# Kernel optimization log

Measured on AMD Instinct MI355X. Metric: run time of the kernel, lower is better.

Reference implementation:

```python
import jax, jax.numpy as jnp
import numpy as np

SCALE = 0.08838834764831845  # 1/sqrt(head_dim=128)


def setup_inputs() -> dict:
    key = jax.random.key(0)
    ks = jax.random.split(key, 5)
    B, H, D = 16, 8, 128          # batch (decode seqs), kv heads, head_dim
    BS, BPS = 16, 128             # block_size, blocks per sequence
    NBLK = B * BPS                # total cache blocks (2048)
    CTX = 2048                    # context length per sequence
    q = jax.random.normal(ks[0], (B, H, D), jnp.float32)
    k = jax.random.normal(ks[1], (B, H, D), jnp.float32)
    v = jax.random.normal(ks[2], (B, H, D), jnp.float32)
    k_cache = jax.random.normal(ks[3], (NBLK, BS, H, D), jnp.float32)
    v_cache = jax.random.normal(ks[4], (NBLK, BS, H, D), jnp.float32)
    # each sequence owns a distinct contiguous set of blocks
    block_tables = jnp.arange(B * BPS, dtype=jnp.int32).reshape(B, BPS)
    context_lens = jnp.full((B,), CTX, dtype=jnp.int32)
    # slot for the newest token (position CTX-1) of each sequence
    last = CTX - 1
    slot_mapping = block_tables[:, last // BS] * BS + (last % BS)
    return {"q": q, "k": k, "v": v, "k_cache": k_cache, "v_cache": v_cache,
            "slot_mapping": slot_mapping.astype(jnp.int32),
            "block_tables": block_tables, "context_lens": context_lens}


def reference(q, k, v, k_cache, v_cache, slot_mapping, block_tables, context_lens):
    # ---- store_kvcache: scatter new k/v tokens into paged caches ----
    nblk, bs, H, D = k_cache.shape
    k_cache = k_cache.reshape(nblk * bs, H, D).at[slot_mapping].set(k).reshape(nblk, bs, H, D)
    v_cache = v_cache.reshape(nblk * bs, H, D).at[slot_mapping].set(v).reshape(nblk, bs, H, D)

    # ---- _sdpa_decode: paged gather + masked attention (q_per_seq = 1) ----
    B, nb = block_tables.shape
    T = nb * bs                              # max tokens per sequence
    token_idx = jnp.arange(T, dtype=jnp.int32)
    block_idx = token_idx // bs
    token_off = token_idx % bs
    block_ids = block_tables[:, block_idx]   # [B, T]
    k_all = k_cache[block_ids, token_off]    # [B, T, H, D]
    v_all = v_cache[block_ids, token_off]    # [B, T, H, D]

    valid = token_idx[None, :] < context_lens[:, None]           # [B, T]
    q_pos = context_lens - 1                                     # q_per_seq == 1
    causal = token_idx[None, :] <= q_pos[:, None]                # [B, T]
    mask = valid & causal

    scores = jnp.einsum("bhd,bthd->bht", q, k_all) * SCALE       # [B, H, T]
    scores = jnp.where(mask[:, None, :], scores, -jnp.inf)
    p = jax.nn.softmax(scores, axis=-1)
    out = jnp.einsum("bht,bthd->bhd", p, v_all)                  # [B, H, D]
    return out
```

## Files before the change

### kernel.cpp

```cpp
#include <hip/hip_runtime.h>
#include <math.h>

#define B_ 16
#define H_ 8
#define D_ 128
#define BS_ 16
#define BPS_ 128
#define T_ (BPS_ * BS_)
#define ROW_ (H_ * D_)
#define SCALE_ 0.08838834764831845f

template<int NS>
__global__ __launch_bounds__(256) void attn_partial(
    const float* __restrict__ q,
    const float* __restrict__ knew,
    const float* __restrict__ vnew,
    const float* __restrict__ kc,
    const float* __restrict__ vc,
    const int* __restrict__ btab,
    const int* __restrict__ clen,
    float* __restrict__ ws_m,
    float* __restrict__ ws_l,
    float* __restrict__ ws_o)
{
    constexpr int CHUNK = T_ / NS;
    constexpr int TPW = CHUNK / 4;
    constexpr int NBLK_C = CHUNK / BS_;

    const int c = blockIdx.x;
    const int b = blockIdx.y;
    const int tid = threadIdx.x;
    const int wave = tid >> 6;
    const int lane = tid & 63;
    const int hl = lane & 31;
    const int half = lane >> 5;
    const int ctx = clen[b];
    const int cs = c * CHUNK;

    __shared__ int   s_bt[NBLK_C];
    __shared__ float s_p[H_][CHUNK];
    __shared__ float s_mx[H_], s_l[H_];
    __shared__ float s_o[4][H_][D_];

    if (tid < NBLK_C) s_bt[tid] = btab[b * BPS_ + c * NBLK_C + tid];

    float4 q4[4];
    #pragma unroll
    for (int j = 0; j < 4; ++j)
        q4[j] = *(const float4*)(q + (size_t)b * ROW_ + j * 256 + half * 128 + 4 * hl);
    __syncthreads();

    #pragma unroll 4
    for (int i = 0; i < TPW; i += 2) {
        float4 k4[8];
        #pragma unroll
        for (int u = 0; u < 2; ++u) {
            const int t = wave * TPW + i + u;
            const int tg = cs + t;
            const int blk = s_bt[t >> 4];
            const float* rb = (tg == ctx - 1)
                ? (knew + (size_t)b * ROW_)
                : (kc + ((size_t)blk * BS_ + (tg & 15)) * ROW_);
            #pragma unroll
            for (int j = 0; j < 4; ++j)
                k4[u * 4 + j] = *(const float4*)(rb + j * 256 + half * 128 + 4 * hl);
        }
        #pragma unroll
        for (int u = 0; u < 2; ++u) {
            const int t = wave * TPW + i + u;
            const int tg = cs + t;
            #pragma unroll
            for (int j = 0; j < 4; ++j) {
                const float4 kv = k4[u * 4 + j];
                float s = q4[j].x * kv.x + q4[j].y * kv.y + q4[j].z * kv.z + q4[j].w * kv.w;
                s += __shfl_xor(s, 16);
                s += __shfl_xor(s, 8);
                s += __shfl_xor(s, 4);
                s += __shfl_xor(s, 2);
                s += __shfl_xor(s, 1);
                if (hl == 0) s_p[2 * j + half][t] = (tg < ctx) ? s * SCALE_ : -INFINITY;
            }
        }
    }
    __syncthreads();

    {
        const int h = tid >> 5;
        float m = -INFINITY;
        for (int t = hl; t < CHUNK; t += 32) m = fmaxf(m, s_p[h][t]);
        m = fmaxf(m, __shfl_xor(m, 16));
        m = fmaxf(m, __shfl_xor(m, 8));
        m = fmaxf(m, __shfl_xor(m, 4));
        m = fmaxf(m, __shfl_xor(m, 2));
        m = fmaxf(m, __shfl_xor(m, 1));
        if (hl == 0) s_mx[h] = fmaxf(m, -1e30f);
    }
    __syncthreads();
    {
        const int h = tid >> 5;
        const float mx = s_mx[h];
        float l = 0.f;
        for (int t = hl; t < CHUNK; t += 32) {
            const float p = __expf(s_p[h][t] - mx);
            s_p[h][t] = p;
            l += p;
        }
        l += __shfl_xor(l, 16);
        l += __shfl_xor(l, 8);
        l += __shfl_xor(l, 4);
        l += __shfl_xor(l, 2);
        l += __shfl_xor(l, 1);
        if (hl == 0) s_l[h] = l;
    }
    __syncthreads();

    float4 acc[4];
    #pragma unroll
    for (int j = 0; j < 4; ++j) acc[j] = make_float4(0.f, 0.f, 0.f, 0.f);
    #pragma unroll 4
    for (int i = 0; i < TPW; i += 2) {
        float4 v4[8];
        #pragma unroll
        for (int u = 0; u < 2; ++u) {
            const int t = wave * TPW + i + u;
            const int tg = cs + t;
            const int blk = s_bt[t >> 4];
            const float* rb = (tg == ctx - 1)
                ? (vnew + (size_t)b * ROW_)
                : (vc + ((size_t)blk * BS_ + (tg & 15)) * ROW_);
            #pragma unroll
            for (int j = 0; j < 4; ++j)
                v4[u * 4 + j] = *(const float4*)(rb + j * 256 + half * 128 + 4 * hl);
        }
        #pragma unroll
        for (int u = 0; u < 2; ++u) {
            const int t = wave * TPW + i + u;
            #pragma unroll
            for (int j = 0; j < 4; ++j) {
                const float pw = s_p[2 * j + half][t];
                acc[j].x += pw * v4[u * 4 + j].x;
                acc[j].y += pw * v4[u * 4 + j].y;
                acc[j].z += pw * v4[u * 4 + j].z;
                acc[j].w += pw * v4[u * 4 + j].w;
            }
        }
    }
    #pragma unroll
    for (int j = 0; j < 4; ++j)
        *(float4*)&s_o[wave][2 * j + half][4 * hl] = acc[j];
    __syncthreads();

    for (int r = tid; r < H_ * D_; r += 256) {
        const int h = r >> 7, d = r & 127;
        const float oo = s_o[0][h][d] + s_o[1][h][d] + s_o[2][h][d] + s_o[3][h][d];
        ws_o[((size_t)(b * H_ + h) * NS + c) * D_ + d] = oo;
    }
    if (tid < H_) {
        ws_m[(b * H_ + tid) * NS + c] = s_mx[tid];
        ws_l[(b * H_ + tid) * NS + c] = s_l[tid];
    }
}

template<int NS>
__global__ __launch_bounds__(128) void attn_reduce(
    const float* __restrict__ ws_m,
    const float* __restrict__ ws_l,
    const float* __restrict__ ws_o,
    float* __restrict__ out)
{
    const int bh = blockIdx.x;
    const int tid = threadIdx.x;

    __shared__ float s_co[NS];
    __shared__ float s_lg;

    if (tid < 64) {
        float m = -INFINITY;
        for (int cc = tid; cc < NS; cc += 64) m = fmaxf(m, ws_m[bh * NS + cc]);
        m = fmaxf(m, __shfl_xor(m, 32));
        m = fmaxf(m, __shfl_xor(m, 16));
        m = fmaxf(m, __shfl_xor(m, 8));
        m = fmaxf(m, __shfl_xor(m, 4));
        m = fmaxf(m, __shfl_xor(m, 2));
        m = fmaxf(m, __shfl_xor(m, 1));
        float lw = 0.f;
        for (int cc = tid; cc < NS; cc += 64) {
            const float co = __expf(ws_m[bh * NS + cc] - m);
            s_co[cc] = co;
            lw += ws_l[bh * NS + cc] * co;
        }
        lw += __shfl_xor(lw, 32);
        lw += __shfl_xor(lw, 16);
        lw += __shfl_xor(lw, 8);
        lw += __shfl_xor(lw, 4);
        lw += __shfl_xor(lw, 2);
        lw += __shfl_xor(lw, 1);
        if (tid == 0) s_lg = lw;
    }
    __syncthreads();

    float acc = 0.f;
    #pragma unroll 8
    for (int cc = 0; cc < NS; ++cc)
        acc += s_co[cc] * ws_o[((size_t)bh * NS + cc) * D_ + tid];
    out[(size_t)bh * D_ + tid] = acc / s_lg;
}

template<int NS>
static void launch_all(const float* q, const float* knew, const float* vnew,
                       const float* kc, const float* vc,
                       const int* btab, const int* clen,
                       float* ws, float* out, hipStream_t stream)
{
    float* ws_m = ws;
    float* ws_l = ws + B_ * H_ * NS;
    float* ws_o = ws + 2 * B_ * H_ * NS;
    attn_partial<NS><<<dim3(NS, B_), 256, 0, stream>>>(q, knew, vnew, kc, vc,
                                                       btab, clen, ws_m, ws_l, ws_o);
    attn_reduce<NS><<<dim3(B_ * H_), 128, 0, stream>>>(ws_m, ws_l, ws_o, out);
}

extern "C" void kernel_launch(void* const* d_in, const int* in_sizes, int n_in,
                              void* d_out, int out_size, void* d_ws, size_t ws_size,
                              hipStream_t stream) {
    const float* q    = (const float*)d_in[0];
    const float* knew = (const float*)d_in[1];
    const float* vnew = (const float*)d_in[2];
    const float* kc   = (const float*)d_in[3];
    const float* vc   = (const float*)d_in[4];
    const int* btab = (const int*)d_in[6];
    const int* clen = (const int*)d_in[7];
    float* out = (float*)d_out;
    float* ws  = (float*)d_ws;

    const size_t need64 = (size_t)B_ * H_ * 64 * (2 + D_) * sizeof(float);
    const size_t need32 = (size_t)B_ * H_ * 32 * (2 + D_) * sizeof(float);
    if (ws_size >= need64)      launch_all<64>(q, knew, vnew, kc, vc, btab, clen, ws, out, stream);
    else if (ws_size >= need32) launch_all<32>(q, knew, vnew, kc, vc, btab, clen, ws, out, stream);
    else                        launch_all<16>(q, knew, vnew, kc, vc, btab, clen, ws, out, stream);
}
```

Baseline: 290.5 us.

## Restructure paged decode attention to keep scores in registers and prefetch V

Remaps threads so each group of 8 lanes owns one head, which shrinks the dot-product shuffle reduction to three steps. Scores now stay in registers and probabilities are recomputed on the fly instead of written back to shared memory. The first V tile is prefetched before the softmax barriers, and the max and sum passes are merged, with fewer barriers overall. It also adds a 128-way split when the workspace allows it and sets an occupancy hint in launch bounds. The cost is higher register pressure from fully unrolled score arrays and direct block-table loads from global memory.

```diff
diff --git a/kernel.cpp b/kernel.cpp
--- a/kernel.cpp
+++ b/kernel.cpp
@@ -11,7 +11,7 @@
 #define SCALE_ 0.08838834764831845f
 
 template<int NS>
-__global__ __launch_bounds__(256) void attn_partial(
+__global__ __launch_bounds__(256, 4) void attn_partial(
     const float* __restrict__ q,
     const float* __restrict__ knew,
     const float* __restrict__ vnew,
@@ -25,135 +25,163 @@
 {
     constexpr int CHUNK = T_ / NS;
     constexpr int TPW = CHUNK / 4;
-    constexpr int NBLK_C = CHUNK / BS_;
+    static_assert(TPW % 4 == 0 || TPW == 4, "TPW multiple of 4");
+    constexpr int NB = TPW / 4;
 
     const int c = blockIdx.x;
     const int b = blockIdx.y;
     const int tid = threadIdx.x;
     const int wave = tid >> 6;
     const int lane = tid & 63;
-    const int hl = lane & 31;
-    const int half = lane >> 5;
+    const int h = lane >> 3;
+    const int e = (lane & 7) * 4;
     const int ctx = clen[b];
     const int cs = c * CHUNK;
-
-    __shared__ int   s_bt[NBLK_C];
-    __shared__ float s_p[H_][CHUNK];
+    const int t0 = wave * TPW;
+
+    __shared__ float s_p[H_][CHUNK + 1];
     __shared__ float s_mx[H_], s_l[H_];
-    __shared__ float s_o[4][H_][D_];
-
-    if (tid < NBLK_C) s_bt[tid] = btab[b * BPS_ + c * NBLK_C + tid];
+    __shared__ float s_o[4][H_ * D_];
 
     float4 q4[4];
     #pragma unroll
-    for (int j = 0; j < 4; ++j)
-        q4[j] = *(const float4*)(q + (size_t)b * ROW_ + j * 256 + half * 128 + 4 * hl);
-    __syncthreads();
-
-    #pragma unroll 4
-    for (int i = 0; i < TPW; i += 2) {
-        float4 k4[8];
-        #pragma unroll
-        for (int u = 0; u < 2; ++u) {
-            const int t = wave * TPW + i + u;
+    for (int i = 0; i < 4; ++i)
+        q4[i] = *(const float4*)(q + (size_t)b * ROW_ + h * 128 + i * 32 + e);
+
+    float sc[TPW];
+
+    #pragma unroll
+    for (int bt = 0; bt < NB; ++bt) {
+        float4 kb[4][4];
+        #pragma unroll
+        for (int u = 0; u < 4; ++u) {
+            const int t = t0 + bt * 4 + u;
             const int tg = cs + t;
-            const int blk = s_bt[t >> 4];
+            const int blk = btab[b * BPS_ + (tg >> 4)];
             const float* rb = (tg == ctx - 1)
                 ? (knew + (size_t)b * ROW_)
-                : (kc + ((size_t)blk * BS_ + (tg & 15)) * ROW_);
-            #pragma unroll
-            for (int j = 0; j < 4; ++j)
-                k4[u * 4 + j] = *(const float4*)(rb + j * 256 + half * 128 + 4 * hl);
-        }
-        #pragma unroll
-        for (int u = 0; u < 2; ++u) {
-            const int t = wave * TPW + i + u;
+                : (kc + ((size_t)blk * BS_ + (t & 15)) * ROW_);
+            #pragma unroll
+            for (int i = 0; i < 4; ++i)
+                kb[u][i] = *(const float4*)(rb + h * 128 + i * 32 + e);
+        }
+        #pragma unroll
+        for (int u = 0; u < 4; ++u) {
+            const int t = t0 + bt * 4 + u;
             const int tg = cs + t;
-            #pragma unroll
-            for (int j = 0; j < 4; ++j) {
-                const float4 kv = k4[u * 4 + j];
-                float s = q4[j].x * kv.x + q4[j].y * kv.y + q4[j].z * kv.z + q4[j].w * kv.w;
-                s += __shfl_xor(s, 16);
-                s += __shfl_xor(s, 8);
-                s += __shfl_xor(s, 4);
-                s += __shfl_xor(s, 2);
-                s += __shfl_xor(s, 1);
-                if (hl == 0) s_p[2 * j + half][t] = (tg < ctx) ? s * SCALE_ : -INFINITY;
-            }
-        }
-    }
-    __syncthreads();
+            float s = 0.f;
+            #pragma unroll
+            for (int i = 0; i < 4; ++i)
+                s += q4[i].x * kb[u][i].x + q4[i].y * kb[u][i].y
+                   + q4[i].z * kb[u][i].z + q4[i].w * kb[u][i].w;
+            s += __shfl_xor(s, 1);
+            s += __shfl_xor(s, 2);
+            s += __shfl_xor(s, 4);
+            s = (tg < ctx) ? s * SCALE_ : -INFINITY;
+            sc[bt * 4 + u] = s;
+            if ((lane & 7) == 0) s_p[h][t] = s;
+        }
+    }
+
+    float4 vb0[4][4];
+    #pragma unroll
+    for (int u = 0; u < 4; ++u) {
+        const int t = t0 + u;
+        const int tg = cs + t;
+        const int blk = btab[b * BPS_ + (tg >> 4)];
+        const float* rb = (tg == ctx - 1)
+            ? (vnew + (size_t)b * ROW_)
+            : (vc + ((size_t)blk * BS_ + (t & 15)) * ROW_);
+        #pragma unroll
+        for (int i = 0; i < 4; ++i)
+            vb0[u][i] = *(const float4*)(rb + h * 128 + i * 32 + e);
+    }
+
+    asm volatile("s_waitcnt lgkmcnt(0)" ::: "memory");
+    __builtin_amdgcn_s_barrier();
+    __builtin_amdgcn_sched_barrier(0);
 
     {
-        const int h = tid >> 5;
+        const int hh = tid >> 5;
+        const int j = tid & 31;
         float m = -INFINITY;
-        for (int t = hl; t < CHUNK; t += 32) m = fmaxf(m, s_p[h][t]);
+        for (int t = j; t < CHUNK; t += 32) m = fmaxf(m, s_p[hh][t]);
         m = fmaxf(m, __shfl_xor(m, 16));
         m = fmaxf(m, __shfl_xor(m, 8));
         m = fmaxf(m, __shfl_xor(m, 4));
         m = fmaxf(m, __shfl_xor(m, 2));
         m = fmaxf(m, __shfl_xor(m, 1));
-        if (hl == 0) s_mx[h] = fmaxf(m, -1e30f);
-    }
-    __syncthreads();
-    {
-        const int h = tid >> 5;
-        const float mx = s_mx[h];
+        m = fmaxf(m, -1e30f);
         float l = 0.f;
-        for (int t = hl; t < CHUNK; t += 32) {
-            const float p = __expf(s_p[h][t] - mx);
-            s_p[h][t] = p;
-            l += p;
-        }
+        for (int t = j; t < CHUNK; t += 32) l += __expf(s_p[hh][t] - m);
         l += __shfl_xor(l, 16);
         l += __shfl_xor(l, 8);
         l += __shfl_xor(l, 4);
         l += __shfl_xor(l, 2);
         l += __shfl_xor(l, 1);
-        if (hl == 0) s_l[h] = l;
-    }
-    __syncthreads();
+        if (j == 0) { s_mx[hh] = m; s_l[hh] = l; }
+    }
+
+    asm volatile("s_waitcnt lgkmcnt(0)" ::: "memory");
+    __builtin_amdgcn_s_barrier();
+    __builtin_amdgcn_sched_barrier(0);
+
+    const float mx = s_mx[h];
 
     float4 acc[4];
     #pragma unroll
-    for (int j = 0; j < 4; ++j) acc[j] = make_float4(0.f, 0.f, 0.f, 0.f);
-    #pragma unroll 4
-    for (int i = 0; i < TPW; i += 2) {
-        float4 v4[8];
-        #pragma unroll
-        for (int u = 0; u < 2; ++u) {
-            const int t = wave * TPW + i + u;
+    for (int i = 0; i < 4; ++i) acc[i] = make_float4(0.f, 0.f, 0.f, 0.f);
+
+    #pragma unroll
+    for (int u = 0; u < 4; ++u) {
+        const float pw = __expf(sc[u] - mx);
+        #pragma unroll
+        for (int i = 0; i < 4; ++i) {
+            acc[i].x += pw * vb0[u][i].x;
+            acc[i].y += pw * vb0[u][i].y;
+            acc[i].z += pw * vb0[u][i].z;
+            acc[i].w += pw * vb0[u][i].w;
+        }
+    }
+    #pragma unroll
+    for (int bt = 1; bt < NB; ++bt) {
+        float4 vb[4][4];
+        #pragma unroll
+        for (int u = 0; u < 4; ++u) {
+            const int t = t0 + bt * 4 + u;
             const int tg = cs + t;
-            const int blk = s_bt[t >> 4];
+            const int blk = btab[b * BPS_ + (tg >> 4)];
             const float* rb = (tg == ctx - 1)
                 ? (vnew + (size_t)b * ROW_)
-                : (vc + ((size_t)blk * BS_ + (tg & 15)) * ROW_);
-            #pragma unroll
-            for (int j = 0; j < 4; ++j)
-                v4[u * 4 + j] = *(const float4*)(rb + j * 256 + half * 128 + 4 * hl);
-        }
-        #pragma unroll
-        for (int u = 0; u < 2; ++u) {
-            const int t = wave * TPW + i + u;
-            #pragma unroll
-            for (int j = 0; j < 4; ++j) {
-                const float pw = s_p[2 * j + half][t];
-                acc[j].x += pw * v4[u * 4 + j].x;
-                acc[j].y += pw * v4[u * 4 + j].y;
-                acc[j].z += pw * v4[u * 4 + j].z;
-                acc[j].w += pw * v4[u * 4 + j].w;
+                : (vc + ((size_t)blk * BS_ + (t & 15)) * ROW_);
+            #pragma unroll
+            for (int i = 0; i < 4; ++i)
+                vb[u][i] = *(const float4*)(rb + h * 128 + i * 32 + e);
+        }
+        #pragma unroll
+        for (int u = 0; u < 4; ++u) {
+            const float pw = __expf(sc[bt * 4 + u] - mx);
+            #pragma unroll
+            for (int i = 0; i < 4; ++i) {
+                acc[i].x += pw * vb[u][i].x;
+                acc[i].y += pw * vb[u][i].y;
+                acc[i].z += pw * vb[u][i].z;
+                acc[i].w += pw * vb[u][i].w;
             }
         }
     }
-    #pragma unroll
-    for (int j = 0; j < 4; ++j)
-        *(float4*)&s_o[wave][2 * j + half][4 * hl] = acc[j];
-    __syncthreads();
+
+    #pragma unroll
+    for (int i = 0; i < 4; ++i)
+        *(float4*)&s_o[wave][h * 128 + i * 32 + e] = acc[i];
+
+    asm volatile("s_waitcnt lgkmcnt(0)" ::: "memory");
+    __builtin_amdgcn_s_barrier();
+    __builtin_amdgcn_sched_barrier(0);
 
     for (int r = tid; r < H_ * D_; r += 256) {
-        const int h = r >> 7, d = r & 127;
-        const float oo = s_o[0][h][d] + s_o[1][h][d] + s_o[2][h][d] + s_o[3][h][d];
-        ws_o[((size_t)(b * H_ + h) * NS + c) * D_ + d] = oo;
+        const float oo = s_o[0][r] + s_o[1][r] + s_o[2][r] + s_o[3][r];
+        ws_o[((size_t)(b * H_ + (r >> 7)) * NS + c) * D_ + (r & 127)] = oo;
     }
     if (tid < H_) {
         ws_m[(b * H_ + tid) * NS + c] = s_mx[tid];
@@ -233,9 +261,11 @@
     float* out = (float*)d_out;
     float* ws  = (float*)d_ws;
 
-    const size_t need64 = (size_t)B_ * H_ * 64 * (2 + D_) * sizeof(float);
-    const size_t need32 = (size_t)B_ * H_ * 32 * (2 + D_) * sizeof(float);
-    if (ws_size >= need64)      launch_all<64>(q, knew, vnew, kc, vc, btab, clen, ws, out, stream);
+    const size_t need128 = (size_t)B_ * H_ * 128 * (2 + D_) * sizeof(float);
+    const size_t need64  = (size_t)B_ * H_ * 64  * (2 + D_) * sizeof(float);
+    const size_t need32  = (size_t)B_ * H_ * 32  * (2 + D_) * sizeof(float);
+    if (ws_size >= need128)     launch_all<128>(q, knew, vnew, kc, vc, btab, clen, ws, out, stream);
+    else if (ws_size >= need64) launch_all<64>(q, knew, vnew, kc, vc, btab, clen, ws, out, stream);
     else if (ws_size >= need32) launch_all<32>(q, knew, vnew, kc, vc, btab, clen, ws, out, stream);
     else                        launch_all<16>(q, knew, vnew, kc, vc, btab, clen, ws, out, stream);
 }
```

Result: slower. 296.7 us (+2.1%).
